# Performance work log

Measured on AMD Instinct MI355X. Metric: run time of the kernel, lower is better.

Reference implementation:

```python
import jax, jax.numpy as jnp
import numpy as np

N1, N2 = 262144, 65536          # dense / coarse point counts (packed batch)
PREV, SKIP, M0, M1 = 512, 256, 256, 256
EPS_BN = 1e-5                    # torch BatchNorm1d default eps
EPS_DIST = 1e-8


def _bn(x, g, b):
    # BatchNorm1d in training mode: biased batch stats over the point axis
    m = x.mean(axis=0)
    v = x.var(axis=0)
    return (x - m) * jax.lax.rsqrt(v + EPS_BN) * g + b


def setup_inputs() -> dict:
    key = jax.random.key(0)
    ks = jax.random.split(key, 8)
    inp = {
        "points1": jax.random.normal(ks[0], (N1, SKIP), jnp.float32),
        "points2": jax.random.normal(ks[1], (N2, PREV), jnp.float32),
        "dist": jax.random.uniform(ks[2], (N1, 3), jnp.float32),
        "idx": jax.random.randint(ks[3], (N1, 3), 0, N2, dtype=jnp.int32),
        # mlp_f0 / norm_f0
        "Wf0": jax.random.normal(ks[4], (PREV, M0), jnp.float32) / np.sqrt(PREV).astype(np.float32),
        "bf0": jnp.zeros((M0,), jnp.float32),
        "gf0": jnp.ones((M0,), jnp.float32),
        "betaf0": jnp.zeros((M0,), jnp.float32),
        # mlp_s0 / norm_s0 (skip path)
        "Ws0": jax.random.normal(ks[5], (SKIP, M0), jnp.float32) / np.sqrt(SKIP).astype(np.float32),
        "bs0": jnp.zeros((M0,), jnp.float32),
        "gs0": jnp.ones((M0,), jnp.float32),
        "betas0": jnp.zeros((M0,), jnp.float32),
        # mlp_convs[0] / mlp_bns[0]
        "W1": jax.random.normal(ks[6], (M0, M1), jnp.float32) / np.sqrt(M0).astype(np.float32),
        "b1": jnp.zeros((M1,), jnp.float32),
        "g1": jnp.ones((M1,), jnp.float32),
        "beta1": jnp.zeros((M1,), jnp.float32),
    }
    return inp


def reference(points1, points2, dist, idx, Wf0, bf0, gf0, betaf0,
              Ws0, bs0, gs0, betas0, W1, b1, g1, beta1):
    # f0 MLP + BN on coarse features: [N2, PREV] -> [N2, M0]
    p2 = _bn(points2 @ Wf0 + bf0, gf0, betaf0)
    # inverse-distance weights over 3 neighbors: [N1, 3]
    dr = 1.0 / (dist + EPS_DIST)
    w = dr / dr.sum(axis=1, keepdims=True)
    # fused gather + weighted sum: p2[idx] is [N1, 3, M0]
    interp = jnp.einsum('nkc,nk->nc', p2[idx], w)
    # skip path: [N1, SKIP] -> [N1, M0]
    skip = _bn(points1 @ Ws0 + bs0, gs0, betas0)
    x = jax.nn.relu(interp + skip)
    # mlp_convs stack (one layer here): Linear + BN + ReLU
    x = jax.nn.relu(_bn(x @ W1 + b1, g1, beta1))
    return x
```

## Files before the change

kernel.cpp:

```cpp
#include <hip/hip_runtime.h>
#include <hip/hip_bf16.h>

#define CN1 262144
#define CN2 65536
#define CPREV 512
#define CSKIP 256

using u16 = unsigned short;

typedef __attribute__((ext_vector_type(8))) short short8;
typedef __attribute__((ext_vector_type(8))) unsigned short ushort8;
typedef __attribute__((ext_vector_type(4))) float f32x4;
typedef __attribute__((ext_vector_type(8))) float f32x8;

__device__ __forceinline__ float toF(float v) { return v; }
__device__ __forceinline__ float toF(u16 u) { return __uint_as_float(((unsigned)u) << 16); }
__device__ __forceinline__ u16 f2bf(float f) {
    unsigned b = __float_as_uint(f);
    b += 0x7FFFu + ((b >> 16) & 1u);
    return (u16)(b >> 16);
}
__device__ __forceinline__ unsigned pack2(float lo, float hi) {
    return ((unsigned)f2bf(hi) << 16) | (unsigned)f2bf(lo);
}

__global__ __launch_bounds__(256) void transpose_all(
    const float* __restrict__ Wf0, const float* __restrict__ Ws0,
    const float* __restrict__ W1,
    u16* __restrict__ Wtf0, u16* __restrict__ Wts0, u16* __restrict__ Wt1)
{
    int b = blockIdx.x;
    const float* W; u16* Wt; int ksh, e;
    if (b < 512)      { W = Wf0; Wt = Wtf0; ksh = 9; e = b * 256 + threadIdx.x; }
    else if (b < 768) { W = Ws0; Wt = Wts0; ksh = 8; e = (b - 512) * 256 + threadIdx.x; }
    else              { W = W1;  Wt = Wt1;  ksh = 8; e = (b - 768) * 256 + threadIdx.x; }
    int K = 1 << ksh;
    int n = e >> ksh;
    int k = e & (K - 1);
    Wt[e] = f2bf(W[((size_t)k << 8) + n]);
}

template<typename OT>
__global__ __launch_bounds__(512) void gemm_mfma(
    const float* __restrict__ Af, const u16* __restrict__ Wt,
    const float* __restrict__ bias, OT* __restrict__ C,
    float* __restrict__ partial, int M, int K)
{
    __shared__ u16 As[128 * 40];
    __shared__ u16 Bs[256 * 40];
    const int t = threadIdx.x;
    const int bm = blockIdx.x * 128;
    const int lane = t & 63;
    const int wid = t >> 6;
    const int wr = wid >> 2;
    const int wc = wid & 3;

    const int arow = t >> 2;
    const int koff = (t & 3) * 8;

    f32x4 acc[4][4] = {};

    float4 ga0, ga1;
    ushort8 gb0, gb1;

    auto LOAD = [&](int k0) {
        const float* p = Af + (size_t)(bm + arow) * K + k0 + koff;
        ga0 = *(const float4*)p;
        ga1 = *(const float4*)(p + 4);
        const u16* q = Wt + (size_t)arow * K + k0 + koff;
        gb0 = *(const ushort8*)q;
        gb1 = *(const ushort8*)(q + (size_t)128 * K);
    };

    const int nk = K >> 5;
    LOAD(0);
    for (int it = 0; it < nk; ++it) {
        __syncthreads();
        {
            uint4 w;
            w.x = pack2(ga0.x, ga0.y);
            w.y = pack2(ga0.z, ga0.w);
            w.z = pack2(ga1.x, ga1.y);
            w.w = pack2(ga1.z, ga1.w);
            *(uint4*)&As[arow * 40 + koff] = w;
        }
        *(ushort8*)&Bs[arow * 40 + koff] = gb0;
        *(ushort8*)&Bs[(128 + arow) * 40 + koff] = gb1;
        __syncthreads();
        if (it + 1 < nk) LOAD((it + 1) << 5);

        const int kq = (lane >> 4) * 8;
        const int rr = lane & 15;
        short8 af[4];
#pragma unroll
        for (int mi = 0; mi < 4; ++mi)
            af[mi] = *(const short8*)&As[(wr * 64 + mi * 16 + rr) * 40 + kq];
#pragma unroll
        for (int ni = 0; ni < 4; ++ni) {
            short8 bf = *(const short8*)&Bs[(wc * 64 + ni * 16 + rr) * 40 + kq];
#pragma unroll
            for (int mi = 0; mi < 4; ++mi)
                acc[mi][ni] = __builtin_amdgcn_mfma_f32_16x16x32_bf16(
                    af[mi], bf, acc[mi][ni], 0, 0, 0);
        }
    }

    __syncthreads();
    float* cs  = (float*)As;
    float* cs2 = ((float*)As) + 512;
    const int r4 = (lane >> 4) * 4;
    const int cc = lane & 15;
#pragma unroll
    for (int ni = 0; ni < 4; ++ni) {
        int col = wc * 64 + ni * 16 + cc;
        float bv = bias[col];
        float s = 0.f, s2 = 0.f;
#pragma unroll
        for (int mi = 0; mi < 4; ++mi) {
            size_t r0 = (size_t)bm + wr * 64 + mi * 16 + r4;
            f32x4 v = acc[mi][ni];
#pragma unroll
            for (int j = 0; j < 4; ++j) {
                float val = v[j] + bv;
                s += val;
                s2 = fmaf(val, val, s2);
                if constexpr (sizeof(OT) == 4)
                    C[(r0 + j) * 256 + col] = val;
                else
                    C[(r0 + j) * 256 + col] = f2bf(val);
            }
        }
        s  += __shfl_xor(s, 16);  s  += __shfl_xor(s, 32);
        s2 += __shfl_xor(s2, 16); s2 += __shfl_xor(s2, 32);
        if (lane < 16) { cs[wr * 256 + col] = s; cs2[wr * 256 + col] = s2; }
    }
    __syncthreads();
    if (t < 256) {
        partial[(size_t)blockIdx.x * 512 + t]       = cs[t] + cs[256 + t];
        partial[(size_t)blockIdx.x * 512 + 256 + t] = cs2[t] + cs2[256 + t];
    }
}

template<typename OT>
__global__ __launch_bounds__(512) void gemm_fused(
    const u16* __restrict__ skipb, const u16* __restrict__ y2,
    const float* __restrict__ dist, const int* __restrict__ idx,
    const float* __restrict__ ssf, const float* __restrict__ sss,
    const u16* __restrict__ Wt, const float* __restrict__ bias,
    OT* __restrict__ C, float* __restrict__ partial)
{
    const int K = 256;
    __shared__ u16 As[128 * 40];
    __shared__ u16 Bs[256 * 40];
    const int t = threadIdx.x;
    const int bm = blockIdx.x * 128;
    const int lane = t & 63;
    const int wid = t >> 6;
    const int wr = wid >> 2;
    const int wc = wid & 3;

    const int arow = t >> 2;
    const int koff = (t & 3) * 8;
    const int row = bm + arow;

    float d0 = dist[row * 3 + 0], d1 = dist[row * 3 + 1], d2 = dist[row * 3 + 2];
    float r0 = 1.f / (d0 + 1e-8f), r1 = 1.f / (d1 + 1e-8f), r2 = 1.f / (d2 + 1e-8f);
    float inv = 1.f / (r0 + r1 + r2);
    const float w0 = r0 * inv, w1 = r1 * inv, w2 = r2 * inv;
    const size_t i0 = (size_t)idx[row * 3 + 0];
    const size_t i1 = (size_t)idx[row * 3 + 1];
    const size_t i2 = (size_t)idx[row * 3 + 2];

    f32x4 acc[4][4] = {};

    ushort8 sk8, a0, a1, a2, gb0, gb1;
    f32x8 sf, sx, csh;

    auto LOAD = [&](int k0) {
        const int kc = k0 + koff;
        sk8 = *(const ushort8*)(skipb + (size_t)row * 256 + kc);
        a0  = *(const ushort8*)(y2 + i0 * 256 + kc);
        a1  = *(const ushort8*)(y2 + i1 * 256 + kc);
        a2  = *(const ushort8*)(y2 + i2 * 256 + kc);
        sf  = *(const f32x8*)(ssf + kc);
        sx  = *(const f32x8*)(sss + kc);
        csh = *(const f32x8*)(sss + 256 + kc);
        const u16* q = Wt + (size_t)arow * K + k0 + koff;
        gb0 = *(const ushort8*)q;
        gb1 = *(const ushort8*)(q + (size_t)128 * K);
    };

    const int nk = K >> 5;
    LOAD(0);
    for (int it = 0; it < nk; ++it) {
        __syncthreads();
        {
            float xs[8];
#pragma unroll
            for (int j = 0; j < 8; ++j) {
                float iv = w0 * toF((u16)a0[j]) + w1 * toF((u16)a1[j])
                         + w2 * toF((u16)a2[j]);
                float val = fmaf(iv, sf[j], fmaf(toF((u16)sk8[j]), sx[j], csh[j]));
                xs[j] = fmaxf(val, 0.f);
            }
            uint4 w;
            w.x = pack2(xs[0], xs[1]);
            w.y = pack2(xs[2], xs[3]);
            w.z = pack2(xs[4], xs[5]);
            w.w = pack2(xs[6], xs[7]);
            *(uint4*)&As[arow * 40 + koff] = w;
        }
        *(ushort8*)&Bs[arow * 40 + koff] = gb0;
        *(ushort8*)&Bs[(128 + arow) * 40 + koff] = gb1;
        __syncthreads();
        if (it + 1 < nk) LOAD((it + 1) << 5);

        const int kq = (lane >> 4) * 8;
        const int rr = lane & 15;
        short8 af[4];
#pragma unroll
        for (int mi = 0; mi < 4; ++mi)
            af[mi] = *(const short8*)&As[(wr * 64 + mi * 16 + rr) * 40 + kq];
#pragma unroll
        for (int ni = 0; ni < 4; ++ni) {
            short8 bf = *(const short8*)&Bs[(wc * 64 + ni * 16 + rr) * 40 + kq];
#pragma unroll
            for (int mi = 0; mi < 4; ++mi)
                acc[mi][ni] = __builtin_amdgcn_mfma_f32_16x16x32_bf16(
                    af[mi], bf, acc[mi][ni], 0, 0, 0);
        }
    }

    __syncthreads();
    float* cs  = (float*)As;
    float* cs2 = ((float*)As) + 512;
    const int r4 = (lane >> 4) * 4;
    const int cc = lane & 15;
#pragma unroll
    for (int ni = 0; ni < 4; ++ni) {
        int col = wc * 64 + ni * 16 + cc;
        float bv = bias[col];
        float s = 0.f, s2 = 0.f;
#pragma unroll
        for (int mi = 0; mi < 4; ++mi) {
            size_t r0 = (size_t)bm + wr * 64 + mi * 16 + r4;
            f32x4 v = acc[mi][ni];
#pragma unroll
            for (int j = 0; j < 4; ++j) {
                float val = v[j] + bv;
                s += val;
                s2 = fmaf(val, val, s2);
                if constexpr (sizeof(OT) == 4)
                    C[(r0 + j) * 256 + col] = val;
                else
                    C[(r0 + j) * 256 + col] = f2bf(val);
            }
        }
        s  += __shfl_xor(s, 16);  s  += __shfl_xor(s, 32);
        s2 += __shfl_xor(s2, 16); s2 += __shfl_xor(s2, 32);
        if (lane < 16) { cs[wr * 256 + col] = s; cs2[wr * 256 + col] = s2; }
    }
    __syncthreads();
    if (t < 256) {
        partial[(size_t)blockIdx.x * 512 + t]       = cs[t] + cs[256 + t];
        partial[(size_t)blockIdx.x * 512 + 256 + t] = cs2[t] + cs2[256 + t];
    }
}

__global__ __launch_bounds__(256) void colstats_final_par(
    const float* __restrict__ partial, int nb, float invR,
    const float* __restrict__ g, const float* __restrict__ beta,
    const float* __restrict__ fold, float* __restrict__ ss)
{
    int c = blockIdx.x;
    int t = threadIdx.x;
    float s = 0.f, s2 = 0.f;
    for (int b = t; b < nb; b += 256) {
        s  += partial[(size_t)b * 512 + c];
        s2 += partial[(size_t)b * 512 + 256 + c];
    }
#pragma unroll
    for (int o = 32; o > 0; o >>= 1) {
        s += __shfl_xor(s, o);
        s2 += __shfl_xor(s2, o);
    }
    __shared__ float rs[4], rs2[4];
    if ((t & 63) == 0) { rs[t >> 6] = s; rs2[t >> 6] = s2; }
    __syncthreads();
    if (t == 0) {
        float S  = rs[0] + rs[1] + rs[2] + rs[3];
        float S2 = rs2[0] + rs2[1] + rs2[2] + rs2[3];
        float m = S * invR;
        float var = fmaf(-m, m, S2 * invR);
        float scale = g[c] * rsqrtf(var + 1e-5f);
        float shift = fmaf(-m, scale, beta[c]);
        if (fold) shift += fold[256 + c];
        ss[c] = scale;
        ss[256 + c] = shift;
    }
}

__global__ __launch_bounds__(256) void bn_relu_cvt(
    const u16* __restrict__ y3, float* __restrict__ out,
    const float* __restrict__ ss)
{
    size_t e = ((size_t)blockIdx.x * 256 + threadIdx.x) * 8;
    int kc = (int)(e & 255);
    ushort8 v = *(const ushort8*)(y3 + e);
    f32x8 sc = *(const f32x8*)(ss + kc);
    f32x8 sh = *(const f32x8*)(ss + 256 + kc);
    float4 o0, o1;
    o0.x = fmaxf(fmaf(toF((u16)v[0]), sc[0], sh[0]), 0.f);
    o0.y = fmaxf(fmaf(toF((u16)v[1]), sc[1], sh[1]), 0.f);
    o0.z = fmaxf(fmaf(toF((u16)v[2]), sc[2], sh[2]), 0.f);
    o0.w = fmaxf(fmaf(toF((u16)v[3]), sc[3], sh[3]), 0.f);
    o1.x = fmaxf(fmaf(toF((u16)v[4]), sc[4], sh[4]), 0.f);
    o1.y = fmaxf(fmaf(toF((u16)v[5]), sc[5], sh[5]), 0.f);
    o1.z = fmaxf(fmaf(toF((u16)v[6]), sc[6], sh[6]), 0.f);
    o1.w = fmaxf(fmaf(toF((u16)v[7]), sc[7], sh[7]), 0.f);
    *(float4*)(out + e) = o0;
    *(float4*)(out + e + 4) = o1;
}

__global__ __launch_bounds__(256) void bn_relu_inplace(
    float* __restrict__ out, const float* __restrict__ ss)
{
    size_t i4 = (size_t)blockIdx.x * 256 + threadIdx.x;
    int c4 = (int)(i4 & 63);
    float4 v = reinterpret_cast<float4*>(out)[i4];
    float4 sc = reinterpret_cast<const float4*>(ss)[c4];
    float4 sh = reinterpret_cast<const float4*>(ss + 256)[c4];
    v.x = fmaxf(fmaf(v.x, sc.x, sh.x), 0.f);
    v.y = fmaxf(fmaf(v.y, sc.y, sh.y), 0.f);
    v.z = fmaxf(fmaf(v.z, sc.z, sh.z), 0.f);
    v.w = fmaxf(fmaf(v.w, sc.w, sh.w), 0.f);
    reinterpret_cast<float4*>(out)[i4] = v;
}

extern "C" void kernel_launch(void* const* d_in, const int* in_sizes, int n_in,
                              void* d_out, int out_size, void* d_ws, size_t ws_size,
                              hipStream_t stream) {
    const float* points1 = (const float*)d_in[0];
    const float* points2 = (const float*)d_in[1];
    const float* dist    = (const float*)d_in[2];
    const int*   idx     = (const int*)d_in[3];
    const float* Wf0     = (const float*)d_in[4];
    const float* bf0     = (const float*)d_in[5];
    const float* gf0     = (const float*)d_in[6];
    const float* betaf0  = (const float*)d_in[7];
    const float* Ws0     = (const float*)d_in[8];
    const float* bs0     = (const float*)d_in[9];
    const float* gs0     = (const float*)d_in[10];
    const float* betas0  = (const float*)d_in[11];
    const float* W1      = (const float*)d_in[12];
    const float* b1      = (const float*)d_in[13];
    const float* g1      = (const float*)d_in[14];
    const float* beta1   = (const float*)d_in[15];

    u16* ws = (u16*)d_ws;
    size_t off = 0;
    u16* y2   = ws + off;  off += (size_t)CN2 * 256;
    u16* xbuf = ws + off;  off += (size_t)CN1 * 256;
    u16* Wtf0 = ws + off;  off += 512 * 256;
    u16* Wts0 = ws + off;  off += 256 * 256;
    u16* Wt1  = ws + off;  off += 256 * 256;
    float* partial = (float*)(ws + off); off += (size_t)2048 * 512 * 2;
    float* ss_f0 = (float*)(ws + off); off += 1024;
    float* ss_s0 = (float*)(ws + off); off += 1024;
    float* ss_1  = (float*)(ws + off); off += 1024;
    u16* y3 = ws + off;
    const size_t NEED = (off + (size_t)CN1 * 256) * 2;
    const bool fused_y3 = (ws_size >= NEED);
    float* out = (float*)d_out;

    transpose_all<<<1024, 256, 0, stream>>>(Wf0, Ws0, W1, Wtf0, Wts0, Wt1);

    gemm_mfma<u16><<<CN2 / 128, 512, 0, stream>>>(
        points2, Wtf0, bf0, y2, partial, CN2, CPREV);
    colstats_final_par<<<256, 256, 0, stream>>>(partial, CN2 / 128, 1.0f / CN2,
                                                gf0, betaf0, nullptr, ss_f0);
    gemm_mfma<u16><<<CN1 / 128, 512, 0, stream>>>(
        points1, Wts0, bs0, xbuf, partial, CN1, CSKIP);
    colstats_final_par<<<256, 256, 0, stream>>>(partial, CN1 / 128, 1.0f / CN1,
                                                gs0, betas0, ss_f0, ss_s0);
    if (fused_y3) {
        gemm_fused<u16><<<CN1 / 128, 512, 0, stream>>>(
            xbuf, y2, dist, idx, ss_f0, ss_s0, Wt1, b1, y3, partial);
    } else {
        gemm_fused<float><<<CN1 / 128, 512, 0, stream>>>(
            xbuf, y2, dist, idx, ss_f0, ss_s0, Wt1, b1, out, partial);
    }
    colstats_final_par<<<256, 256, 0, stream>>>(partial, CN1 / 128, 1.0f / CN1,
                                                g1, beta1, nullptr, ss_1);
    if (fused_y3) {
        bn_relu_cvt<<<32768, 256, 0, stream>>>(y3, out, ss_1);
    } else {
        bn_relu_inplace<<<CN1 / 4, 256, 0, stream>>>(out, ss_1);
    }
}
```

Baseline: 490.9 us.

## Double-buffer global prefetch, stage BN tables in LDS, coalesce epilogue stores

Both GEMM kernels now prefetch two K-tiles ahead into double-buffered registers instead of one, to hide more global and gather latency. The fused kernel keeps the BN scale/shift tables in shared memory instead of reloading them from global memory every iteration. A shared epilogue routes accumulator tiles through an LDS patch so each thread writes 16-byte row-contiguous stores instead of scattered scalar stores. The cost is more registers per thread, which may lower occupancy, plus extra barriers in the epilogue.

```diff
diff --git a/kernel.cpp b/kernel.cpp
--- a/kernel.cpp
+++ b/kernel.cpp
@@ -41,6 +41,81 @@
 }
 
 template<typename OT>
+__device__ __forceinline__ void epilogue(
+    f32x4 (&acc)[4][4], u16* AsU, u16* BsU,
+    const float* __restrict__ bias, OT* __restrict__ C,
+    float* __restrict__ partial, int bm, int t)
+{
+    const int lane = t & 63;
+    const int wid = t >> 6;
+    const int wr = wid >> 2;
+    const int wc = wid & 3;
+    __syncthreads();
+    float* cs  = (float*)AsU;
+    float* cs2 = ((float*)AsU) + 512;
+    float* patch = ((float*)BsU) + wid * (16 * 36);
+    const int r4 = (lane >> 4) * 4;
+    const int cc = lane & 15;
+    float bv[4];
+#pragma unroll
+    for (int ni = 0; ni < 4; ++ni) bv[ni] = bias[wc * 64 + ni * 16 + cc];
+
+#pragma unroll
+    for (int ni = 0; ni < 4; ++ni) {
+        int col = wc * 64 + ni * 16 + cc;
+        float s = 0.f, s2 = 0.f;
+#pragma unroll
+        for (int mi = 0; mi < 4; ++mi) {
+#pragma unroll
+            for (int j = 0; j < 4; ++j) {
+                float val = acc[mi][ni][j] + bv[ni];
+                s += val;
+                s2 = fmaf(val, val, s2);
+            }
+        }
+        s  += __shfl_xor(s, 16);  s  += __shfl_xor(s, 32);
+        s2 += __shfl_xor(s2, 16); s2 += __shfl_xor(s2, 32);
+        if (lane < 16) { cs[wr * 256 + col] = s; cs2[wr * 256 + col] = s2; }
+    }
+
+    const int trow = lane >> 2;
+    const int c8 = (lane & 3) * 8;
+#pragma unroll
+    for (int mi = 0; mi < 4; ++mi) {
+#pragma unroll
+        for (int np = 0; np < 2; ++np) {
+            __syncthreads();
+#pragma unroll
+            for (int h = 0; h < 2; ++h) {
+                int ni = np * 2 + h;
+#pragma unroll
+                for (int j = 0; j < 4; ++j)
+                    patch[(r4 + j) * 36 + h * 16 + cc] = acc[mi][ni][j] + bv[ni];
+            }
+            __syncthreads();
+            float4 v0 = *(float4*)&patch[trow * 36 + c8];
+            float4 v1 = *(float4*)&patch[trow * 36 + c8 + 4];
+            size_t r = (size_t)bm + wr * 64 + mi * 16 + trow;
+            size_t cb = (size_t)wc * 64 + np * 32 + c8;
+            if constexpr (sizeof(OT) == 4) {
+                *(float4*)((float*)C + r * 256 + cb) = v0;
+                *(float4*)((float*)C + r * 256 + cb + 4) = v1;
+            } else {
+                uint4 p;
+                p.x = pack2(v0.x, v0.y); p.y = pack2(v0.z, v0.w);
+                p.z = pack2(v1.x, v1.y); p.w = pack2(v1.z, v1.w);
+                *(uint4*)((u16*)C + r * 256 + cb) = p;
+            }
+        }
+    }
+    __syncthreads();
+    if (t < 256) {
+        partial[(size_t)blockIdx.x * 512 + t]       = cs[t] + cs[256 + t];
+        partial[(size_t)blockIdx.x * 512 + 256 + t] = cs2[t] + cs2[256 + t];
+    }
+}
+
+template<typename OT>
 __global__ __launch_bounds__(512) void gemm_mfma(
     const float* __restrict__ Af, const u16* __restrict__ Wt,
     const float* __restrict__ bias, OT* __restrict__ C,
@@ -60,34 +135,36 @@
 
     f32x4 acc[4][4] = {};
 
-    float4 ga0, ga1;
-    ushort8 gb0, gb1;
-
-    auto LOAD = [&](int k0) {
+    float4 ga0[2], ga1[2];
+    ushort8 gb0[2], gb1[2];
+
+    auto LOAD = [&](int k0, int b) {
         const float* p = Af + (size_t)(bm + arow) * K + k0 + koff;
-        ga0 = *(const float4*)p;
-        ga1 = *(const float4*)(p + 4);
+        ga0[b] = *(const float4*)p;
+        ga1[b] = *(const float4*)(p + 4);
         const u16* q = Wt + (size_t)arow * K + k0 + koff;
-        gb0 = *(const ushort8*)q;
-        gb1 = *(const ushort8*)(q + (size_t)128 * K);
+        gb0[b] = *(const ushort8*)q;
+        gb1[b] = *(const ushort8*)(q + (size_t)128 * K);
     };
 
     const int nk = K >> 5;
-    LOAD(0);
+    LOAD(0, 0);
+    LOAD(32, 1);
     for (int it = 0; it < nk; ++it) {
+        const int b = it & 1;
         __syncthreads();
         {
             uint4 w;
-            w.x = pack2(ga0.x, ga0.y);
-            w.y = pack2(ga0.z, ga0.w);
-            w.z = pack2(ga1.x, ga1.y);
-            w.w = pack2(ga1.z, ga1.w);
+            w.x = pack2(ga0[b].x, ga0[b].y);
+            w.y = pack2(ga0[b].z, ga0[b].w);
+            w.z = pack2(ga1[b].x, ga1[b].y);
+            w.w = pack2(ga1[b].z, ga1[b].w);
             *(uint4*)&As[arow * 40 + koff] = w;
         }
-        *(ushort8*)&Bs[arow * 40 + koff] = gb0;
-        *(ushort8*)&Bs[(128 + arow) * 40 + koff] = gb1;
+        *(ushort8*)&Bs[arow * 40 + koff] = gb0[b];
+        *(ushort8*)&Bs[(128 + arow) * 40 + koff] = gb1[b];
         __syncthreads();
-        if (it + 1 < nk) LOAD((it + 1) << 5);
+        if (it + 2 < nk) LOAD((it + 2) << 5, b);
 
         const int kq = (lane >> 4) * 8;
         const int rr = lane & 15;
@@ -105,40 +182,7 @@
         }
     }
 
-    __syncthreads();
-    float* cs  = (float*)As;
-    float* cs2 = ((float*)As) + 512;
-    const int r4 = (lane >> 4) * 4;
-    const int cc = lane & 15;
-#pragma unroll
-    for (int ni = 0; ni < 4; ++ni) {
-        int col = wc * 64 + ni * 16 + cc;
-        float bv = bias[col];
-        float s = 0.f, s2 = 0.f;
-#pragma unroll
-        for (int mi = 0; mi < 4; ++mi) {
-            size_t r0 = (size_t)bm + wr * 64 + mi * 16 + r4;
-            f32x4 v = acc[mi][ni];
-#pragma unroll
-            for (int j = 0; j < 4; ++j) {
-                float val = v[j] + bv;
-                s += val;
-                s2 = fmaf(val, val, s2);
-                if constexpr (sizeof(OT) == 4)
-                    C[(r0 + j) * 256 + col] = val;
-                else
-                    C[(r0 + j) * 256 + col] = f2bf(val);
-            }
-        }
-        s  += __shfl_xor(s, 16);  s  += __shfl_xor(s, 32);
-        s2 += __shfl_xor(s2, 16); s2 += __shfl_xor(s2, 32);
-        if (lane < 16) { cs[wr * 256 + col] = s; cs2[wr * 256 + col] = s2; }
-    }
-    __syncthreads();
-    if (t < 256) {
-        partial[(size_t)blockIdx.x * 512 + t]       = cs[t] + cs[256 + t];
-        partial[(size_t)blockIdx.x * 512 + 256 + t] = cs2[t] + cs2[256 + t];
-    }
+    epilogue<OT>(acc, As, Bs, bias, C, partial, bm, t);
 }
 
 template<typename OT>
@@ -152,6 +196,7 @@
     const int K = 256;
     __shared__ u16 As[128 * 40];
     __shared__ u16 Bs[256 * 40];
+    __shared__ float sstab[768];
     const int t = threadIdx.x;
     const int bm = blockIdx.x * 128;
     const int lane = t & 63;
@@ -162,6 +207,9 @@
     const int arow = t >> 2;
     const int koff = (t & 3) * 8;
     const int row = bm + arow;
+
+    for (int e = t; e < 768; e += 512)
+        sstab[e] = (e < 256) ? ssf[e] : sss[e - 256];
 
     float d0 = dist[row * 3 + 0], d1 = dist[row * 3 + 1], d2 = dist[row * 3 + 2];
     float r0 = 1.f / (d0 + 1e-8f), r1 = 1.f / (d1 + 1e-8f), r2 = 1.f / (d2 + 1e-8f);
@@ -173,34 +221,36 @@
 
     f32x4 acc[4][4] = {};
 
-    ushort8 sk8, a0, a1, a2, gb0, gb1;
-    f32x8 sf, sx, csh;
-
-    auto LOAD = [&](int k0) {
+    ushort8 sk8[2], a0[2], a1[2], a2[2], gb0[2], gb1[2];
+
+    auto LOADG = [&](int k0, int b) {
         const int kc = k0 + koff;
-        sk8 = *(const ushort8*)(skipb + (size_t)row * 256 + kc);
-        a0  = *(const ushort8*)(y2 + i0 * 256 + kc);
-        a1  = *(const ushort8*)(y2 + i1 * 256 + kc);
-        a2  = *(const ushort8*)(y2 + i2 * 256 + kc);
-        sf  = *(const f32x8*)(ssf + kc);
-        sx  = *(const f32x8*)(sss + kc);
-        csh = *(const f32x8*)(sss + 256 + kc);
-        const u16* q = Wt + (size_t)arow * K + k0 + koff;
-        gb0 = *(const ushort8*)q;
-        gb1 = *(const ushort8*)(q + (size_t)128 * K);
+        sk8[b] = *(const ushort8*)(skipb + (size_t)row * 256 + kc);
+        a0[b]  = *(const ushort8*)(y2 + i0 * 256 + kc);
+        a1[b]  = *(const ushort8*)(y2 + i1 * 256 + kc);
+        a2[b]  = *(const ushort8*)(y2 + i2 * 256 + kc);
+        const u16* q = Wt + (size_t)arow * K + kc;
+        gb0[b] = *(const ushort8*)q;
+        gb1[b] = *(const ushort8*)(q + (size_t)128 * K);
     };
 
     const int nk = K >> 5;
-    LOAD(0);
+    LOADG(0, 0);
+    LOADG(32, 1);
     for (int it = 0; it < nk; ++it) {
+        const int b = it & 1;
         __syncthreads();
         {
+            const int kc = (it << 5) + koff;
+            f32x8 sf = *(const f32x8*)&sstab[kc];
+            f32x8 sx = *(const f32x8*)&sstab[256 + kc];
+            f32x8 ch = *(const f32x8*)&sstab[512 + kc];
             float xs[8];
 #pragma unroll
             for (int j = 0; j < 8; ++j) {
-                float iv = w0 * toF((u16)a0[j]) + w1 * toF((u16)a1[j])
-                         + w2 * toF((u16)a2[j]);
-                float val = fmaf(iv, sf[j], fmaf(toF((u16)sk8[j]), sx[j], csh[j]));
+                float iv = w0 * toF((u16)a0[b][j]) + w1 * toF((u16)a1[b][j])
+                         + w2 * toF((u16)a2[b][j]);
+                float val = fmaf(iv, sf[j], fmaf(toF((u16)sk8[b][j]), sx[j], ch[j]));
                 xs[j] = fmaxf(val, 0.f);
             }
             uint4 w;
@@ -210,10 +260,10 @@
             w.w = pack2(xs[6], xs[7]);
             *(uint4*)&As[arow * 40 + koff] = w;
         }
-        *(ushort8*)&Bs[arow * 40 + koff] = gb0;
-        *(ushort8*)&Bs[(128 + arow) * 40 + koff] = gb1;
+        *(ushort8*)&Bs[arow * 40 + koff] = gb0[b];
+        *(ushort8*)&Bs[(128 + arow) * 40 + koff] = gb1[b];
         __syncthreads();
-        if (it + 1 < nk) LOAD((it + 1) << 5);
+        if (it + 2 < nk) LOADG((it + 2) << 5, b);
 
         const int kq = (lane >> 4) * 8;
         const int rr = lane & 15;
@@ -231,40 +281,7 @@
         }
     }
 
-    __syncthreads();
-    float* cs  = (float*)As;
-    float* cs2 = ((float*)As) + 512;
-    const int r4 = (lane >> 4) * 4;
-    const int cc = lane & 15;
-#pragma unroll
-    for (int ni = 0; ni < 4; ++ni) {
-        int col = wc * 64 + ni * 16 + cc;
-        float bv = bias[col];
-        float s = 0.f, s2 = 0.f;
-#pragma unroll
-        for (int mi = 0; mi < 4; ++mi) {
-            size_t r0 = (size_t)bm + wr * 64 + mi * 16 + r4;
-            f32x4 v = acc[mi][ni];
-#pragma unroll
-            for (int j = 0; j < 4; ++j) {
-                float val = v[j] + bv;
-                s += val;
-                s2 = fmaf(val, val, s2);
-                if constexpr (sizeof(OT) == 4)
-                    C[(r0 + j) * 256 + col] = val;
-                else
-                    C[(r0 + j) * 256 + col] = f2bf(val);
-            }
-        }
-        s  += __shfl_xor(s, 16);  s  += __shfl_xor(s, 32);
-        s2 += __shfl_xor(s2, 16); s2 += __shfl_xor(s2, 32);
-        if (lane < 16) { cs[wr * 256 + col] = s; cs2[wr * 256 + col] = s2; }
-    }
-    __syncthreads();
-    if (t < 256) {
-        partial[(size_t)blockIdx.x * 512 + t]       = cs[t] + cs[256 + t];
-        partial[(size_t)blockIdx.x * 512 + 256 + t] = cs2[t] + cs2[256 + t];
-    }
+    epilogue<OT>(acc, As, Bs, bias, C, partial, bm, t);
 }
 
 __global__ __launch_bounds__(256) void colstats_final_par(
```

Measured after the change: 811.0 us. 65.2% more time.
